# Optimization experiments

Hardware: AMD Instinct MI355X
Metric: run time of the kernel (lower is better)

## Reference

```python
import jax, jax.numpy as jnp
import numpy as np

B, T, D, H = 512, 512, 128, 128


def setup_inputs() -> dict:
    key = jax.random.key(0)
    k1, k2, k3 = jax.random.split(key, 3)
    bound = 1.0 / np.sqrt(D)  # kaiming_uniform with a=sqrt(5) on [D,H]
    inp = {
        "input": jax.random.normal(k1, (B, T, D), dtype=jnp.float32),
        "mask": jnp.ones((B, T), dtype=jnp.int32),
        "Wt": jax.random.uniform(k2, (D, H), jnp.float32, -bound, bound),
        "Wx": jax.random.uniform(k3, (D, H), jnp.float32, -bound, bound),
        "rate": jnp.zeros((1,), jnp.float32) + 0.8,
    }
    return inp


def reference(input, mask, Wt, Wx, rate):
    b, t, d = input.shape
    # time decays: [t-1, t-2, ..., 0] + 1  -> shape [t]
    b_time_decays = jnp.arange(t - 1, -1, -1, dtype=input.dtype) + 1.0  # [T]

    # get_last_visit: pick features at last valid (mask==1) timestep per batch
    last_idx = jnp.sum(mask, axis=1).astype(jnp.int32) - 1            # [B]
    last_visit = jnp.take_along_axis(input, last_idx[:, None, None], axis=1)[:, 0]  # [B,D]

    q = last_visit @ Wt                                   # [B,H]
    k = jnp.einsum('btd,dh->bth', input, Wx)              # [B,T,H]
    dot_product = jnp.einsum('bh,bth->bt', q, k)          # [B,T]

    sig = jax.nn.sigmoid(dot_product)
    denominator = jax.nn.sigmoid(rate) * (
        jnp.log(2.72 + (1.0 - sig)) * b_time_decays[None, :]
    )
    e = jax.nn.relu(sig / denominator)

    e = jnp.where(mask == 0, -1e9, e)
    a = jax.nn.softmax(e, axis=1)                         # [B,T]
    v = jnp.einsum('bt,btd->bd', a, input)                # [B,D]
    return v, a
```

## Files before the change

### kernel.cpp

```cpp
#include <hip/hip_runtime.h>
#include <math.h>

constexpr int Bn = 512;
constexpr int Tn = 512;
constexpr int Dn = 128;
constexpr int Hn = 128;
constexpr int NT = 512;
constexpr int NW = NT / 64;

typedef float f4 __attribute__((ext_vector_type(4)));

__device__ __forceinline__ float rowsum16(float x) {
    int v;
    v = __float_as_int(x);
    x += __int_as_float(__builtin_amdgcn_update_dpp(0, v, 0x121, 0xF, 0xF, true));
    v = __float_as_int(x);
    x += __int_as_float(__builtin_amdgcn_update_dpp(0, v, 0x122, 0xF, 0xF, true));
    v = __float_as_int(x);
    x += __int_as_float(__builtin_amdgcn_update_dpp(0, v, 0x124, 0xF, 0xF, true));
    v = __float_as_int(x);
    x += __int_as_float(__builtin_amdgcn_update_dpp(0, v, 0x128, 0xF, 0xF, true));
    return x;
}

__global__ __launch_bounds__(NT, 4)
void single_attn_fused_nt(const float* __restrict__ input,
                          const int*   __restrict__ mask,
                          const float* __restrict__ Wt,
                          const float* __restrict__ Wx,
                          const float* __restrict__ rate,
                          float* __restrict__ out_v,
                          float* __restrict__ out_a)
{
    const int b    = blockIdx.x;
    const int tid  = threadIdx.x;
    const int lane = tid & 63;
    const int wid  = tid >> 6;
    const int seg  = tid & 15;
    const int rg   = tid >> 4;
    const float* __restrict__ inb = input + (size_t)b * Tn * Dn;
    const f4* __restrict__ in4 = (const f4*)inb;

    __shared__ float ps[Tn];
    __shared__ int   msk[Tn];
    __shared__ float lv[Dn];
    __shared__ float qs[Hn];
    __shared__ float us[Dn];
    __shared__ float redl[NW];
    __shared__ int   ired[NW];
    __shared__ float vp[32 * 132];

    const int mv = mask[(size_t)b * Tn + tid];
    msk[tid] = mv;
    {
        int ms = mv;
        #pragma unroll
        for (int off = 32; off > 0; off >>= 1) ms += __shfl_down(ms, off, 64);
        if (lane == 0) ired[wid] = ms;
    }
    __syncthreads();
    int last_idx;
    {
        int s = 0;
        #pragma unroll
        for (int w = 0; w < NW; ++w) s += ired[w];
        last_idx = s - 1;
    }
    if (tid < Dn) lv[tid] = inb[(size_t)last_idx * Dn + tid];
    __syncthreads();
    if (tid < Hn) {
        float a0 = 0.f, a1 = 0.f;
        #pragma unroll 16
        for (int d0 = 0; d0 < Dn; d0 += 2) {
            a0 = fmaf(lv[d0],     Wt[d0 * Hn + tid],       a0);
            a1 = fmaf(lv[d0 + 1], Wt[(d0 + 1) * Hn + tid], a1);
        }
        qs[tid] = a0 + a1;
    }
    __syncthreads();
    if (tid < Dn) {
        float a0 = 0.f, a1 = 0.f;
        const float* wxr = Wx + tid * Hn;
        #pragma unroll 16
        for (int h = 0; h < Hn; h += 2) {
            a0 = fmaf(wxr[h],     qs[h],     a0);
            a1 = fmaf(wxr[h + 1], qs[h + 1], a1);
        }
        us[tid] = a0 + a1;
    }
    __syncthreads();

    const float srate = 1.f / (1.f + __expf(-rate[0]));
    const f4 u4a = ((const f4*)us)[seg * 2];
    const f4 u4b = ((const f4*)us)[seg * 2 + 1];

    f4 v0 = (f4)(0.f);
    f4 v1 = (f4)(0.f);
    float lsum = 0.f;

    #pragma unroll 8
    for (int it = 0; it < 16; ++it) {
        const int row = it * 32 + rg;
        const f4 x0 = __builtin_nontemporal_load(&in4[row * 32 + seg * 2]);
        const f4 x1 = __builtin_nontemporal_load(&in4[row * 32 + seg * 2 + 1]);
        float dot = x0.x * u4a.x + x0.y * u4a.y + x0.z * u4a.z + x0.w * u4a.w;
        dot = fmaf(x1.x, u4b.x, dot);
        dot = fmaf(x1.y, u4b.y, dot);
        dot = fmaf(x1.z, u4b.z, dot);
        dot = fmaf(x1.w, u4b.w, dot);
        dot = rowsum16(dot);
        const float sig = 1.f / (1.f + __expf(-dot));
        const float den = srate * (__logf(2.72f + (1.f - sig)) * (float)(Tn - row));
        const float e   = fmaxf(sig / den, 0.f);
        const float p   = msk[row] ? __expf(e) : 0.f;
        v0 += p * x0;
        v1 += p * x1;
        if (seg == 0) { ps[row] = p; lsum += p; }
    }

    {
        float* vr = vp + rg * 132 + seg * 8;
        ((f4*)vr)[0] = v0;
        ((f4*)vr)[1] = v1;
    }
    float ls = lsum;
    #pragma unroll
    for (int off = 32; off > 0; off >>= 1) ls += __shfl_down(ls, off, 64);
    if (lane == 0) redl[wid] = ls;
    __syncthreads();

    float l = 0.f;
    #pragma unroll
    for (int w = 0; w < NW; ++w) l += redl[w];
    const float inv_l = 1.f / l;

    out_a[(size_t)b * Tn + tid] = ps[tid] * inv_l;

    if (tid < Dn) {
        float s = 0.f;
        #pragma unroll
        for (int r = 0; r < 32; ++r) s += vp[r * 132 + tid];
        out_v[(size_t)b * Dn + tid] = s * inv_l;
    }
}

extern "C" void kernel_launch(void* const* d_in, const int* in_sizes, int n_in,
                              void* d_out, int out_size, void* d_ws, size_t ws_size,
                              hipStream_t stream) {
    const float* input = (const float*)d_in[0];
    const int*   mask  = (const int*)d_in[1];
    const float* Wt    = (const float*)d_in[2];
    const float* Wx    = (const float*)d_in[3];
    const float* rate  = (const float*)d_in[4];

    float* out   = (float*)d_out;
    float* out_v = out;
    float* out_a = out + Bn * Dn;

    single_attn_fused_nt<<<Bn, NT, 0, stream>>>(input, mask, Wt, Wx, rate, out_v, out_a);
}
```

Baseline: 33.30 us.

## Map each row to 32 lanes with one float4 load and raise occupancy

Changes the thread-to-data mapping so each 128-float row is covered by 32 lanes, each doing one float4 load, instead of 16 lanes doing two. The row reduction gains a ds_swizzle step, the partial-v buffer in shared memory is halved, and the main loop runs 32 iterations. The nontemporal load hint is dropped and launch bounds rise to 6 blocks per CU, aiming at lower register and LDS pressure and more memory-level parallelism. The cost is twice as many iterations, each with an extra cross-lane step, and possibly fewer loads in flight per thread.

```diff
diff --git a/kernel.cpp b/kernel.cpp
--- a/kernel.cpp
+++ b/kernel.cpp
@@ -22,22 +22,27 @@
     x += __int_as_float(__builtin_amdgcn_update_dpp(0, v, 0x128, 0xF, 0xF, true));
     return x;
 }
+__device__ __forceinline__ float rowsum32(float x) {
+    x = rowsum16(x);
+    x += __int_as_float(__builtin_amdgcn_ds_swizzle(__float_as_int(x), 0x401F));
+    return x;
+}
 
-__global__ __launch_bounds__(NT, 4)
-void single_attn_fused_nt(const float* __restrict__ input,
-                          const int*   __restrict__ mask,
-                          const float* __restrict__ Wt,
-                          const float* __restrict__ Wx,
-                          const float* __restrict__ rate,
-                          float* __restrict__ out_v,
-                          float* __restrict__ out_a)
+__global__ __launch_bounds__(NT, 6)
+void single_attn_fused5(const float* __restrict__ input,
+                        const int*   __restrict__ mask,
+                        const float* __restrict__ Wt,
+                        const float* __restrict__ Wx,
+                        const float* __restrict__ rate,
+                        float* __restrict__ out_v,
+                        float* __restrict__ out_a)
 {
     const int b    = blockIdx.x;
     const int tid  = threadIdx.x;
     const int lane = tid & 63;
     const int wid  = tid >> 6;
-    const int seg  = tid & 15;
-    const int rg   = tid >> 4;
+    const int c32  = lane & 31;
+    const int rh   = lane >> 5;
     const float* __restrict__ inb = input + (size_t)b * Tn * Dn;
     const f4* __restrict__ in4 = (const f4*)inb;
 
@@ -48,7 +53,7 @@
     __shared__ float us[Dn];
     __shared__ float redl[NW];
     __shared__ int   ired[NW];
-    __shared__ float vp[32 * 132];
+    __shared__ float vp[16 * 132];
 
     const int mv = mask[(size_t)b * Tn + tid];
     msk[tid] = mv;
@@ -91,37 +96,30 @@
     __syncthreads();
 
     const float srate = 1.f / (1.f + __expf(-rate[0]));
-    const f4 u4a = ((const f4*)us)[seg * 2];
-    const f4 u4b = ((const f4*)us)[seg * 2 + 1];
+    const f4 u4 = ((const f4*)us)[c32];
 
-    f4 v0 = (f4)(0.f);
-    f4 v1 = (f4)(0.f);
+    f4 vacc = (f4)(0.f);
     float lsum = 0.f;
 
     #pragma unroll 8
-    for (int it = 0; it < 16; ++it) {
-        const int row = it * 32 + rg;
-        const f4 x0 = __builtin_nontemporal_load(&in4[row * 32 + seg * 2]);
-        const f4 x1 = __builtin_nontemporal_load(&in4[row * 32 + seg * 2 + 1]);
-        float dot = x0.x * u4a.x + x0.y * u4a.y + x0.z * u4a.z + x0.w * u4a.w;
-        dot = fmaf(x1.x, u4b.x, dot);
-        dot = fmaf(x1.y, u4b.y, dot);
-        dot = fmaf(x1.z, u4b.z, dot);
-        dot = fmaf(x1.w, u4b.w, dot);
-        dot = rowsum16(dot);
+    for (int it = 0; it < 32; ++it) {
+        const int row = it * 16 + wid * 2 + rh;
+        const f4 x = in4[row * 32 + c32];
+        float dot = x.x * u4.x + x.y * u4.y;
+        dot = fmaf(x.z, u4.z, dot);
+        dot = fmaf(x.w, u4.w, dot);
+        dot = rowsum32(dot);
         const float sig = 1.f / (1.f + __expf(-dot));
         const float den = srate * (__logf(2.72f + (1.f - sig)) * (float)(Tn - row));
         const float e   = fmaxf(sig / den, 0.f);
         const float p   = msk[row] ? __expf(e) : 0.f;
-        v0 += p * x0;
-        v1 += p * x1;
-        if (seg == 0) { ps[row] = p; lsum += p; }
+        vacc += p * x;
+        if (c32 == 0) { ps[row] = p; lsum += p; }
     }
 
     {
-        float* vr = vp + rg * 132 + seg * 8;
-        ((f4*)vr)[0] = v0;
-        ((f4*)vr)[1] = v1;
+        float* vr = vp + (wid * 2 + rh) * 132 + c32 * 4;
+        *((f4*)vr) = vacc;
     }
     float ls = lsum;
     #pragma unroll
@@ -139,7 +137,7 @@
     if (tid < Dn) {
         float s = 0.f;
         #pragma unroll
-        for (int r = 0; r < 32; ++r) s += vp[r * 132 + tid];
+        for (int r = 0; r < 16; ++r) s += vp[r * 132 + tid];
         out_v[(size_t)b * Dn + tid] = s * inv_l;
     }
 }
@@ -157,5 +155,5 @@
     float* out_v = out;
     float* out_a = out + Bn * Dn;
 
-    single_attn_fused_nt<<<Bn, NT, 0, stream>>>(input, mask, Wt, Wx, rate, out_v, out_a);
+    single_attn_fused5<<<Bn, NT, 0, stream>>>(input, mask, Wt, Wx, rate, out_v, out_a);
 }
```

Measured after the change: 37.23 us. 11.8% more time.
